# Kernel optimization log

Measured on AMD Instinct MI355X. Metric: run time of the kernel, lower is better.

Reference implementation:

```python
import jax, jax.numpy as jnp
import numpy as np

B, C, H, W = 8, 64, 32, 32
NEG = 256
TEMP = 2.0
FACTOR = 0.8
EPS = 1e-8


def setup_inputs() -> dict:
    key = jax.random.key(0)
    k1, k2, k3, k4 = jax.random.split(key, 4)
    views_1 = jax.random.normal(k1, (B, C, H, W), dtype=jnp.float32)
    views_2 = jax.random.normal(k2, (B, C, H, W), dtype=jnp.float32)
    img = jax.random.uniform(k3, (1, 3, H, W), dtype=jnp.float32)
    neg_idx = jax.random.randint(k4, (B, 2, H * W, NEG), 0, H, dtype=jnp.int32)
    return {"views_1": views_1, "views_2": views_2, "img": img, "neg_idx": neg_idx}


def _forward(views_1, views_2, img, neg_idx):
    hw = H * W
    height = jnp.arange(hw) // W
    width = jnp.arange(hw) % W
    coords = jnp.stack([height, width]).astype(jnp.float32)  # [2, hw]
    img0 = img[0]  # [3, H, W]; original uses img[0] for EVERY batch element
    euc_norm = jnp.sqrt(jnp.asarray((H - 1) ** 2 + (W - 1) ** 2, jnp.float32))
    sqrt3 = jnp.sqrt(jnp.asarray(3.0, jnp.float32))

    center = img0[:, height, width]  # [3, hw]

    def per_sample(z1, z2, nidx):
        # nidx: [2, hw, neg]
        nf = nidx.astype(jnp.float32)
        # torch.norm with no dim => scalar Frobenius norm over [2, neg] per pixel
        d = coords[:, :, None] - nf  # [2, hw, neg]
        euc = jnp.sqrt(jnp.sum(d * d, axis=(0, 2))) / euc_norm  # [hw]
        negs = img0[:, nidx[0], nidx[1]]  # [3, hw, neg]
        rd = center[:, :, None] - negs
        rgb = jnp.sqrt(jnp.sum(rd * rd, axis=(0, 2))) / sqrt3  # [hw]
        weight = euc * FACTOR + rgb * (1.0 - FACTOR)  # [hw], constant across neg

        z1v = z1.reshape(C, hw)  # [c, hw]
        pn = z2[:, nidx[0], nidx[1]]  # [c, hw, neg]
        dot = jnp.einsum('cp,cpn->pn', z1v, pn)  # [hw, neg]
        z1sq = jnp.sum(z1v * z1v, axis=0)  # [hw]
        z1n = jnp.sqrt(z1sq)
        pnn = jnp.sqrt(jnp.sum(pn * pn, axis=0))  # [hw, neg]
        cos = dot / jnp.maximum(z1n[:, None] * pnn, EPS)  # [hw, neg]
        cos0 = z1sq / jnp.maximum(z1sq, EPS)  # [hw] (self-similarity ~ 1)

        sim_neg = jnp.minimum(jnp.abs(cos * weight[:, None]), 1.0)  # [hw, neg]
        sim0 = jnp.minimum(jnp.abs(cos0), 1.0)  # [hw]
        sim = jnp.concatenate(
            [jnp.mean(sim0)[None], jnp.mean(sim_neg, axis=0) / TEMP]
        )  # [neg+1]

        # BCELoss with target = [1, 0, ..., 0]; torch clamps log terms at -100
        logp = jnp.maximum(jnp.log(sim[0]), -100.0)
        log1m = jnp.maximum(jnp.log1p(-sim[1:]), -100.0)
        bce = -(logp + jnp.sum(log1m)) / (NEG + 1)
        return bce, sim

    bce, sims = jax.vmap(per_sample)(views_1, views_2, neg_idx)
    loss = jnp.mean(bce)
    sim_all = jnp.sum(sims, axis=0)
    return (loss, sim_all[0] / B, jnp.sum(sim_all[1:]) / NEG * TEMP / B)


def reference(views_1, views_2, img, neg_idx):
    return _forward(views_1, views_2, img, neg_idx)
```

## Files before the change

### kernel.cpp

```cpp
#include <hip/hip_runtime.h>
#include <math.h>

#define BB 8
#define CC 64
#define HH 32
#define WW 32
#define HW 1024
#define NEGN 256
#define TEMP 2.0f
#define FACTOR 0.8f
#define EPSF 1e-8f

typedef short bf16x8 __attribute__((ext_vector_type(8)));
typedef float f32x4  __attribute__((ext_vector_type(4)));

__device__ inline unsigned short f2bf(float f) {
    unsigned u = __float_as_uint(f);
    u += 0x7FFFu + ((u >> 16) & 1u);
    return (unsigned short)(u >> 16);
}


__global__ __launch_bounds__(256) void prep(
    const float* __restrict__ z1,
    const float* __restrict__ z2,
    const float* __restrict__ img,
    const int*   __restrict__ nidx,
    ushort2* __restrict__ qp,
    float* __restrict__ weight_g,
    unsigned short* __restrict__ z1t,
    unsigned short* __restrict__ z2t,
    float* __restrict__ z1n_ws,
    float* __restrict__ normq_ws,
    float* __restrict__ sim0Part)
{
    __shared__ float imgs_l[3 * HW];
    __shared__ float ctile[64 * 16];
    __shared__ float csq[16];

    const int t   = threadIdx.x;
    const int blk = blockIdx.x;

    const int b_w  = blk >> 7;
    const int p0_8 = (blk & 127) * 8;
    const int lane32 = t & 31;
    const int pp_w   = t >> 5;
    const int p_w    = p0_8 + pp_w;

    const bool isZ1 = (blk < 512);
    const int cvt   = isZ1 ? blk : blk - 512;
    const int b_c   = cvt >> 6;
    const int p0c   = (cvt & 63) * 16;
    const float* __restrict__ src = isZ1 ? z1 : z2;

    const size_t nbase = ((size_t)(b_w * 2) * HW + p_w) * NEGN;
    const int2* __restrict__ nr = reinterpret_cast<const int2*>(nidx + nbase);
    const int2* __restrict__ nc =
        reinterpret_cast<const int2*>(nidx + nbase + (size_t)HW * NEGN);
    int2 rrv[4], ccv[4];
    #pragma unroll
    for (int j = 0; j < 4; ++j) {
        rrv[j] = nr[lane32 + 32 * j];
        ccv[j] = nc[lane32 + 32 * j];
    }

    {
        const float4* __restrict__ imgf4 = reinterpret_cast<const float4*>(img);
        float4* imgs4 = reinterpret_cast<float4*>(imgs_l);
        #pragma unroll
        for (int j = 0; j < 3; ++j) imgs4[t + 256 * j] = imgf4[t + 256 * j];
    }
    {
        #pragma unroll
        for (int i = 0; i < 4; ++i) {
            const int idx = t + 256 * i;
            const int c = idx >> 4, row = idx & 15;
            ctile[idx] = src[((size_t)(b_c * CC + c)) * HW + p0c + row];
        }
    }
    __syncthreads();

    {
        const float cen0 = imgs_l[p_w], cen1 = imgs_l[HW + p_w], cen2 = imgs_l[2 * HW + p_w];
        const float hp = (float)(p_w >> 5), wp = (float)(p_w & 31);

        int q[8];
        #pragma unroll
        for (int j = 0; j < 4; ++j) {
            q[2 * j]     = rrv[j].x * WW + ccv[j].x;
            q[2 * j + 1] = rrv[j].y * WW + ccv[j].y;
        }
        float g0[8], g1[8], g2[8];
        #pragma unroll
        for (int e = 0; e < 8; ++e) {
            g0[e] = imgs_l[q[e]];
            g1[e] = imgs_l[HW + q[e]];
            g2[e] = imgs_l[2 * HW + q[e]];
        }
        float se = 0.f, sr = 0.f;
        #pragma unroll
        for (int j = 0; j < 4; ++j) {
            {
                const float dh = hp - (float)rrv[j].x, dw = wp - (float)ccv[j].x;
                se += dh * dh + dw * dw;
                const float d0 = cen0 - g0[2 * j];
                const float d1 = cen1 - g1[2 * j];
                const float d2 = cen2 - g2[2 * j];
                sr += d0 * d0 + d1 * d1 + d2 * d2;
            }
            {
                const float dh = hp - (float)rrv[j].y, dw = wp - (float)ccv[j].y;
                se += dh * dh + dw * dw;
                const float d0 = cen0 - g0[2 * j + 1];
                const float d1 = cen1 - g1[2 * j + 1];
                const float d2 = cen2 - g2[2 * j + 1];
                sr += d0 * d0 + d1 * d1 + d2 * d2;
            }
        }
        #pragma unroll
        for (int off = 16; off; off >>= 1) {
            se += __shfl_xor(se, off);
            sr += __shfl_xor(sr, off);
        }
        const float euc_norm = sqrtf((float)((HH - 1) * (HH - 1) + (WW - 1) * (WW - 1)));
        const float weight = sqrtf(se) / euc_norm * FACTOR +
                             sqrtf(sr) / sqrtf(3.0f) * (1.0f - FACTOR);

        ushort2* qrow = qp + (size_t)(b_w * 1024 + p0_8) * 128;
        #pragma unroll
        for (int j = 0; j < 4; ++j)
            qrow[pp_w * 128 + lane32 + 32 * j] =
                make_ushort2((unsigned short)q[2 * j], (unsigned short)q[2 * j + 1]);
        if (lane32 == 0) weight_g[b_w * 1024 + p_w] = weight;
    }

    if (t < 16) {
        float s = 0.f;
        #pragma unroll
        for (int c = 0; c < CC; ++c) { const float v = ctile[c * 16 + t]; s += v * v; }
        if (isZ1) {
            z1n_ws[b_c * 1024 + p0c + t] = sqrtf(s);
            csq[t] = fminf(fabsf(s / fmaxf(s, EPSF)), 1.0f);
        } else {
            normq_ws[b_c * 1024 + p0c + t] = sqrtf(s);
        }
    }
    __syncthreads();
    if (isZ1 && t == 0) {
        float s0 = 0.f;
        #pragma unroll
        for (int i = 0; i < 16; ++i) s0 += csq[i];
        sim0Part[cvt] = s0;
    }

    {
        unsigned short* dst =
            (isZ1 ? z1t : z2t) + ((size_t)(b_c * 1024) + p0c) * 64;
        ushort4 pk;
        const int o = 4 * t;
        pk.x = f2bf(ctile[((o + 0) & 63) * 16 + ((o + 0) >> 6)]);
        pk.y = f2bf(ctile[((o + 1) & 63) * 16 + ((o + 1) >> 6)]);
        pk.z = f2bf(ctile[((o + 2) & 63) * 16 + ((o + 2) >> 6)]);
        pk.w = f2bf(ctile[((o + 3) & 63) * 16 + ((o + 3) >> 6)]);
        *reinterpret_cast<ushort4*>(dst + o) = pk;
    }
}

__global__ __launch_bounds__(256, 2) void gemm_mfma(
    const unsigned short* __restrict__ z1t,
    const unsigned short* __restrict__ z2t,
    const float* __restrict__ z1n_ws,
    const float* __restrict__ normq_ws,
    const ushort2* __restrict__ qp,
    const float* __restrict__ weight_g,
    float* __restrict__ simPart)
{
    __shared__ float Dt_s[16 * HW];
    __shared__ float nq_s[HW];
    __shared__ float z1n_s[16];

    const int t    = threadIdx.x;
    const int blk  = blockIdx.x;
    const int b    = blk >> 6;
    const int p0   = (blk & 63) * 16;
    const int wave = t >> 6;
    const int lane = t & 63;
    const int ln15 = lane & 15;
    const int lg   = lane >> 4;

    reinterpret_cast<float4*>(nq_s)[t] =
        reinterpret_cast<const float4*>(normq_ws + b * 1024)[t];
    if (t < 16) z1n_s[t] = z1n_ws[b * 1024 + p0 + t];

    const unsigned short* arow =
        z1t + ((size_t)(b * 1024) + p0 + ln15) * 64 + lg * 8;
    const bf16x8 a0 = *reinterpret_cast<const bf16x8*>(arow);
    const bf16x8 a1 = *reinterpret_cast<const bf16x8*>(arow + 32);

    __syncthreads();

    const int qw = wave * 256;
    #pragma unroll 4
    for (int tile = 0; tile < 16; ++tile) {
        const int q0 = qw + tile * 16;
        const unsigned short* brow =
            z2t + ((size_t)(b * 1024) + q0 + ln15) * 64 + lg * 8;
        const bf16x8 b0 = *reinterpret_cast<const bf16x8*>(brow);
        const bf16x8 b1 = *reinterpret_cast<const bf16x8*>(brow + 32);
        f32x4 acc = {0.f, 0.f, 0.f, 0.f};
        acc = __builtin_amdgcn_mfma_f32_16x16x32_bf16(a0, b0, acc, 0, 0, 0);
        acc = __builtin_amdgcn_mfma_f32_16x16x32_bf16(a1, b1, acc, 0, 0, 0);

        const float pn = nq_s[q0 + ln15];
        #pragma unroll
        for (int i = 0; i < 4; ++i) {
            const int row = lg * 4 + i;
            Dt_s[row * HW + q0 + ln15] = acc[i] / fmaxf(z1n_s[row] * pn, EPSF);
        }
    }

    const int p_b = t >> 4;
    const int tn  = t & 15;
    const ushort2* qrow = qp + (size_t)(b * 1024 + p0 + p_b) * 128;
    ushort2 qv[8];
    #pragma unroll
    for (int j = 0; j < 8; ++j) qv[j] = qrow[tn + 16 * j];
    const float weight = weight_g[b * 1024 + p0 + p_b];
    __syncthreads();

    float2 sv[8];
    #pragma unroll
    for (int j = 0; j < 8; ++j) {
        const float c0 = Dt_s[p_b * HW + qv[j].x];
        const float c1 = Dt_s[p_b * HW + qv[j].y];
        sv[j].x = fminf(fabsf(c0 * weight), 1.0f);
        sv[j].y = fminf(fabsf(c1 * weight), 1.0f);
    }
    __syncthreads();

    float2* simpart2 = reinterpret_cast<float2*>(Dt_s);
    #pragma unroll
    for (int j = 0; j < 8; ++j)
        simpart2[p_b * (NEGN / 2) + tn + 16 * j] = sv[j];
    __syncthreads();

    float s = 0.f;
    #pragma unroll
    for (int pp = 0; pp < 16; ++pp) s += Dt_s[pp * NEGN + t];
    simPart[(size_t)blk * NEGN + t] = s;
}

__global__ __launch_bounds__(256) void reduce_out(
    const float* __restrict__ simPart,
    const float* __restrict__ sim0Part,
    float* __restrict__ out)
{
    const int b = blockIdx.x;
    const int t = threadIdx.x;

    float a = 0.f;
    #pragma unroll 8
    for (int pblk = 0; pblk < 64; ++pblk)
        a += simPart[((size_t)(b * 64 + pblk)) * NEGN + t];

    const float s = a * (1.0f / HW) * (1.0f / TEMP);
    float ssum = s;
    float lsum = fmaxf(log1pf(-s), -100.0f);

    __shared__ float rs[4], rl[4];
    __shared__ float s0sh;
    #pragma unroll
    for (int off = 32; off; off >>= 1) {
        ssum += __shfl_down(ssum, off);
        lsum += __shfl_down(lsum, off);
    }
    if ((t & 63) == 0) { rs[t >> 6] = ssum; rl[t >> 6] = lsum; }

    if (t < 64) {
        float v = sim0Part[b * 64 + t];
        #pragma unroll
        for (int off = 32; off; off >>= 1) v += __shfl_xor(v, off);
        if (t == 0) s0sh = v * (1.0f / HW);
    }
    __syncthreads();

    if (t == 0) {
        const float S = rs[0] + rs[1] + rs[2] + rs[3];
        const float L = rl[0] + rl[1] + rl[2] + rl[3];
        const float s0 = s0sh;
        const float logp = fmaxf(logf(s0), -100.0f);
        atomicAdd(out + 0, -(logp + L) / ((float)(NEGN + 1) * (float)BB));
        atomicAdd(out + 1, s0 / (float)BB);
        atomicAdd(out + 2, S / (float)NEGN * TEMP / (float)BB);
    }
}

extern "C" void kernel_launch(void* const* d_in, const int* in_sizes, int n_in,
                              void* d_out, int out_size, void* d_ws, size_t ws_size,
                              hipStream_t stream) {
    const float* v1   = (const float*)d_in[0];
    const float* v2   = (const float*)d_in[1];
    const float* img  = (const float*)d_in[2];
    const int*   nidx = (const int*)  d_in[3];

    float*   simPart  = (float*)d_ws;
    float*   sim0Part = simPart + 512 * NEGN;
    float*   weight_g = sim0Part + 512;
    float*   z1n_ws   = weight_g + 8192;
    float*   normq_ws = z1n_ws + 8192;
    ushort2* qp       = (ushort2*)(normq_ws + 8192);
    unsigned short* z1t = (unsigned short*)(qp + 1048576);
    unsigned short* z2t = z1t + 8 * 1024 * 64;

    prep<<<1024, 256, 0, stream>>>(v1, v2, img, nidx, qp, weight_g,
                                   z1t, z2t, z1n_ws, normq_ws, sim0Part);
    gemm_mfma<<<512, 256, 0, stream>>>(z1t, z2t, z1n_ws, normq_ws,
                                       qp, weight_g, simPart);
    reduce_out<<<BB, 256, 0, stream>>>(simPart, sim0Part, (float*)d_out);
}
```

Baseline: 91.35 us.

## Fuse z1 prep, weight computation and final reduction into GEMM kernel

The prep kernel now only converts z2 to bf16 and computes its norms. The z1 conversion, the per-pixel distance and color weight computation from the neighbor indices, and the final loss reduction all move into the GEMM kernel. The reduction uses a last-block-done atomic counter per batch, which removes one launch and the qp/weight/z1t workspace round-trips. In exchange the GEMM kernel does more work per block and needs more registers (16 index loads held across the MFMA loop), which may reduce occupancy.

```diff
diff --git a/kernel.cpp b/kernel.cpp
--- a/kernel.cpp
+++ b/kernel.cpp
@@ -21,163 +21,63 @@
 }
 
 
-__global__ __launch_bounds__(256) void prep(
+__global__ __launch_bounds__(256) void prep_z2(
+    const float* __restrict__ z2,
+    unsigned short* __restrict__ z2t,
+    float* __restrict__ normq_ws,
+    unsigned* __restrict__ cnt)
+{
+    __shared__ float ctile[64 * 16];
+
+    const int t   = threadIdx.x;
+    const int blk = blockIdx.x;
+    const int b   = blk >> 6;
+    const int q0  = (blk & 63) * 16;
+
+    if (blk == 0 && t < 8) cnt[t] = 0;
+
+    #pragma unroll
+    for (int i = 0; i < 4; ++i) {
+        const int idx = t + 256 * i;
+        const int c = idx >> 4, row = idx & 15;
+        ctile[idx] = z2[((size_t)(b * CC + c)) * HW + q0 + row];
+    }
+    __syncthreads();
+
+    if (t < 16) {
+        float s = 0.f;
+        #pragma unroll
+        for (int c = 0; c < CC; ++c) { const float v = ctile[c * 16 + t]; s += v * v; }
+        normq_ws[b * 1024 + q0 + t] = sqrtf(s);
+    }
+
+    unsigned short* dst = z2t + ((size_t)(b * 1024) + q0) * 64;
+    ushort4 pk;
+    const int o = 4 * t;
+    pk.x = f2bf(ctile[((o + 0) & 63) * 16 + ((o + 0) >> 6)]);
+    pk.y = f2bf(ctile[((o + 1) & 63) * 16 + ((o + 1) >> 6)]);
+    pk.z = f2bf(ctile[((o + 2) & 63) * 16 + ((o + 2) >> 6)]);
+    pk.w = f2bf(ctile[((o + 3) & 63) * 16 + ((o + 3) >> 6)]);
+    *reinterpret_cast<ushort4*>(dst + o) = pk;
+}
+
+__global__ __launch_bounds__(256, 2) void gemm_fused(
     const float* __restrict__ z1,
-    const float* __restrict__ z2,
     const float* __restrict__ img,
     const int*   __restrict__ nidx,
-    ushort2* __restrict__ qp,
-    float* __restrict__ weight_g,
-    unsigned short* __restrict__ z1t,
-    unsigned short* __restrict__ z2t,
-    float* __restrict__ z1n_ws,
-    float* __restrict__ normq_ws,
-    float* __restrict__ sim0Part)
-{
-    __shared__ float imgs_l[3 * HW];
-    __shared__ float ctile[64 * 16];
-    __shared__ float csq[16];
-
-    const int t   = threadIdx.x;
-    const int blk = blockIdx.x;
-
-    const int b_w  = blk >> 7;
-    const int p0_8 = (blk & 127) * 8;
-    const int lane32 = t & 31;
-    const int pp_w   = t >> 5;
-    const int p_w    = p0_8 + pp_w;
-
-    const bool isZ1 = (blk < 512);
-    const int cvt   = isZ1 ? blk : blk - 512;
-    const int b_c   = cvt >> 6;
-    const int p0c   = (cvt & 63) * 16;
-    const float* __restrict__ src = isZ1 ? z1 : z2;
-
-    const size_t nbase = ((size_t)(b_w * 2) * HW + p_w) * NEGN;
-    const int2* __restrict__ nr = reinterpret_cast<const int2*>(nidx + nbase);
-    const int2* __restrict__ nc =
-        reinterpret_cast<const int2*>(nidx + nbase + (size_t)HW * NEGN);
-    int2 rrv[4], ccv[4];
-    #pragma unroll
-    for (int j = 0; j < 4; ++j) {
-        rrv[j] = nr[lane32 + 32 * j];
-        ccv[j] = nc[lane32 + 32 * j];
-    }
-
-    {
-        const float4* __restrict__ imgf4 = reinterpret_cast<const float4*>(img);
-        float4* imgs4 = reinterpret_cast<float4*>(imgs_l);
-        #pragma unroll
-        for (int j = 0; j < 3; ++j) imgs4[t + 256 * j] = imgf4[t + 256 * j];
-    }
-    {
-        #pragma unroll
-        for (int i = 0; i < 4; ++i) {
-            const int idx = t + 256 * i;
-            const int c = idx >> 4, row = idx & 15;
-            ctile[idx] = src[((size_t)(b_c * CC + c)) * HW + p0c + row];
-        }
-    }
-    __syncthreads();
-
-    {
-        const float cen0 = imgs_l[p_w], cen1 = imgs_l[HW + p_w], cen2 = imgs_l[2 * HW + p_w];
-        const float hp = (float)(p_w >> 5), wp = (float)(p_w & 31);
-
-        int q[8];
-        #pragma unroll
-        for (int j = 0; j < 4; ++j) {
-            q[2 * j]     = rrv[j].x * WW + ccv[j].x;
-            q[2 * j + 1] = rrv[j].y * WW + ccv[j].y;
-        }
-        float g0[8], g1[8], g2[8];
-        #pragma unroll
-        for (int e = 0; e < 8; ++e) {
-            g0[e] = imgs_l[q[e]];
-            g1[e] = imgs_l[HW + q[e]];
-            g2[e] = imgs_l[2 * HW + q[e]];
-        }
-        float se = 0.f, sr = 0.f;
-        #pragma unroll
-        for (int j = 0; j < 4; ++j) {
-            {
-                const float dh = hp - (float)rrv[j].x, dw = wp - (float)ccv[j].x;
-                se += dh * dh + dw * dw;
-                const float d0 = cen0 - g0[2 * j];
-                const float d1 = cen1 - g1[2 * j];
-                const float d2 = cen2 - g2[2 * j];
-                sr += d0 * d0 + d1 * d1 + d2 * d2;
-            }
-            {
-                const float dh = hp - (float)rrv[j].y, dw = wp - (float)ccv[j].y;
-                se += dh * dh + dw * dw;
-                const float d0 = cen0 - g0[2 * j + 1];
-                const float d1 = cen1 - g1[2 * j + 1];
-                const float d2 = cen2 - g2[2 * j + 1];
-                sr += d0 * d0 + d1 * d1 + d2 * d2;
-            }
-        }
-        #pragma unroll
-        for (int off = 16; off; off >>= 1) {
-            se += __shfl_xor(se, off);
-            sr += __shfl_xor(sr, off);
-        }
-        const float euc_norm = sqrtf((float)((HH - 1) * (HH - 1) + (WW - 1) * (WW - 1)));
-        const float weight = sqrtf(se) / euc_norm * FACTOR +
-                             sqrtf(sr) / sqrtf(3.0f) * (1.0f - FACTOR);
-
-        ushort2* qrow = qp + (size_t)(b_w * 1024 + p0_8) * 128;
-        #pragma unroll
-        for (int j = 0; j < 4; ++j)
-            qrow[pp_w * 128 + lane32 + 32 * j] =
-                make_ushort2((unsigned short)q[2 * j], (unsigned short)q[2 * j + 1]);
-        if (lane32 == 0) weight_g[b_w * 1024 + p_w] = weight;
-    }
-
-    if (t < 16) {
-        float s = 0.f;
-        #pragma unroll
-        for (int c = 0; c < CC; ++c) { const float v = ctile[c * 16 + t]; s += v * v; }
-        if (isZ1) {
-            z1n_ws[b_c * 1024 + p0c + t] = sqrtf(s);
-            csq[t] = fminf(fabsf(s / fmaxf(s, EPSF)), 1.0f);
-        } else {
-            normq_ws[b_c * 1024 + p0c + t] = sqrtf(s);
-        }
-    }
-    __syncthreads();
-    if (isZ1 && t == 0) {
-        float s0 = 0.f;
-        #pragma unroll
-        for (int i = 0; i < 16; ++i) s0 += csq[i];
-        sim0Part[cvt] = s0;
-    }
-
-    {
-        unsigned short* dst =
-            (isZ1 ? z1t : z2t) + ((size_t)(b_c * 1024) + p0c) * 64;
-        ushort4 pk;
-        const int o = 4 * t;
-        pk.x = f2bf(ctile[((o + 0) & 63) * 16 + ((o + 0) >> 6)]);
-        pk.y = f2bf(ctile[((o + 1) & 63) * 16 + ((o + 1) >> 6)]);
-        pk.z = f2bf(ctile[((o + 2) & 63) * 16 + ((o + 2) >> 6)]);
-        pk.w = f2bf(ctile[((o + 3) & 63) * 16 + ((o + 3) >> 6)]);
-        *reinterpret_cast<ushort4*>(dst + o) = pk;
-    }
-}
-
-__global__ __launch_bounds__(256, 2) void gemm_mfma(
-    const unsigned short* __restrict__ z1t,
     const unsigned short* __restrict__ z2t,
-    const float* __restrict__ z1n_ws,
     const float* __restrict__ normq_ws,
-    const ushort2* __restrict__ qp,
-    const float* __restrict__ weight_g,
-    float* __restrict__ simPart)
+    float* __restrict__ simPart,
+    float* __restrict__ sim0Part,
+    unsigned* __restrict__ cnt,
+    float* __restrict__ out)
 {
     __shared__ float Dt_s[16 * HW];
-    __shared__ float nq_s[HW];
+    __shared__ float aux[3 * HW];
     __shared__ float z1n_s[16];
+    __shared__ float z1sq_s[16];
+    __shared__ float rs[4], rl[4];
+    __shared__ int   isLast;
 
     const int t    = threadIdx.x;
     const int blk  = blockIdx.x;
@@ -188,51 +88,116 @@
     const int ln15 = lane & 15;
     const int lg   = lane >> 4;
 
+    const int p_b = t >> 4;
+    const int tn  = t & 15;
+    const size_t nbase = ((size_t)(b * 2) * HW + p0 + p_b) * NEGN;
+    const int2* __restrict__ nr = reinterpret_cast<const int2*>(nidx + nbase);
+    const int2* __restrict__ nc =
+        reinterpret_cast<const int2*>(nidx + nbase + (size_t)HW * NEGN);
+    int2 rrv[8], ccv[8];
+    #pragma unroll
+    for (int j = 0; j < 8; ++j) {
+        rrv[j] = nr[tn + 16 * j];
+        ccv[j] = nc[tn + 16 * j];
+    }
+
+    float* nq_s  = aux;
+    float* ctile = aux + HW;
     reinterpret_cast<float4*>(nq_s)[t] =
         reinterpret_cast<const float4*>(normq_ws + b * 1024)[t];
-    if (t < 16) z1n_s[t] = z1n_ws[b * 1024 + p0 + t];
-
-    const unsigned short* arow =
-        z1t + ((size_t)(b * 1024) + p0 + ln15) * 64 + lg * 8;
-    const bf16x8 a0 = *reinterpret_cast<const bf16x8*>(arow);
-    const bf16x8 a1 = *reinterpret_cast<const bf16x8*>(arow + 32);
-
+    #pragma unroll
+    for (int i = 0; i < 4; ++i) {
+        const int idx = t + 256 * i;
+        const int c = idx >> 4, row = idx & 15;
+        ctile[idx] = z1[((size_t)(b * CC + c)) * HW + p0 + row];
+    }
+    __syncthreads();
+
+    if (t < 16) {
+        float s = 0.f;
+        #pragma unroll
+        for (int c = 0; c < CC; ++c) { const float v = ctile[c * 16 + t]; s += v * v; }
+        z1sq_s[t] = s; z1n_s[t] = sqrtf(s);
+    }
+    bf16x8 a0, a1;
+    #pragma unroll
+    for (int j = 0; j < 8; ++j) {
+        a0[j] = (short)f2bf(ctile[(lg * 8 + j) * 16 + ln15]);
+        a1[j] = (short)f2bf(ctile[(32 + lg * 8 + j) * 16 + ln15]);
+    }
     __syncthreads();
 
     const int qw = wave * 256;
     #pragma unroll 4
     for (int tile = 0; tile < 16; ++tile) {
-        const int q0 = qw + tile * 16;
+        const int q0t = qw + tile * 16;
         const unsigned short* brow =
-            z2t + ((size_t)(b * 1024) + q0 + ln15) * 64 + lg * 8;
+            z2t + ((size_t)(b * 1024) + q0t + ln15) * 64 + lg * 8;
         const bf16x8 b0 = *reinterpret_cast<const bf16x8*>(brow);
         const bf16x8 b1 = *reinterpret_cast<const bf16x8*>(brow + 32);
         f32x4 acc = {0.f, 0.f, 0.f, 0.f};
         acc = __builtin_amdgcn_mfma_f32_16x16x32_bf16(a0, b0, acc, 0, 0, 0);
         acc = __builtin_amdgcn_mfma_f32_16x16x32_bf16(a1, b1, acc, 0, 0, 0);
 
-        const float pn = nq_s[q0 + ln15];
+        const float pn = nq_s[q0t + ln15];
         #pragma unroll
         for (int i = 0; i < 4; ++i) {
             const int row = lg * 4 + i;
-            Dt_s[row * HW + q0 + ln15] = acc[i] / fmaxf(z1n_s[row] * pn, EPSF);
+            Dt_s[row * HW + q0t + ln15] = acc[i] / fmaxf(z1n_s[row] * pn, EPSF);
         }
     }
-
-    const int p_b = t >> 4;
-    const int tn  = t & 15;
-    const ushort2* qrow = qp + (size_t)(b * 1024 + p0 + p_b) * 128;
-    ushort2 qv[8];
-    #pragma unroll
-    for (int j = 0; j < 8; ++j) qv[j] = qrow[tn + 16 * j];
-    const float weight = weight_g[b * 1024 + p0 + p_b];
-    __syncthreads();
+    __syncthreads();
+
+    {
+        const float4* __restrict__ imgf4 = reinterpret_cast<const float4*>(img);
+        float4* imgs4 = reinterpret_cast<float4*>(aux);
+        #pragma unroll
+        for (int j = 0; j < 3; ++j) imgs4[t + 256 * j] = imgf4[t + 256 * j];
+    }
+    __syncthreads();
+    float* imgs_l = aux;
+
+    const int pg = p0 + p_b;
+    const float cen0 = imgs_l[pg], cen1 = imgs_l[HW + pg], cen2 = imgs_l[2 * HW + pg];
+    const float hp = (float)(pg >> 5), wp = (float)(pg & 31);
+
+    int qv[16];
+    float se = 0.f, sr = 0.f;
+    #pragma unroll
+    for (int j = 0; j < 8; ++j) {
+        {
+            const int q = rrv[j].x * WW + ccv[j].x; qv[2 * j] = q;
+            const float dh = hp - (float)rrv[j].x, dw = wp - (float)ccv[j].x;
+            se += dh * dh + dw * dw;
+            const float d0 = cen0 - imgs_l[q];
+            const float d1 = cen1 - imgs_l[HW + q];
+            const float d2 = cen2 - imgs_l[2 * HW + q];
+            sr += d0 * d0 + d1 * d1 + d2 * d2;
+        }
+        {
+            const int q = rrv[j].y * WW + ccv[j].y; qv[2 * j + 1] = q;
+            const float dh = hp - (float)rrv[j].y, dw = wp - (float)ccv[j].y;
+            se += dh * dh + dw * dw;
+            const float d0 = cen0 - imgs_l[q];
+            const float d1 = cen1 - imgs_l[HW + q];
+            const float d2 = cen2 - imgs_l[2 * HW + q];
+            sr += d0 * d0 + d1 * d1 + d2 * d2;
+        }
+    }
+    #pragma unroll
+    for (int off = 8; off; off >>= 1) {
+        se += __shfl_xor(se, off);
+        sr += __shfl_xor(sr, off);
+    }
+    const float euc_norm = sqrtf((float)((HH - 1) * (HH - 1) + (WW - 1) * (WW - 1)));
+    const float weight = sqrtf(se) / euc_norm * FACTOR +
+                         sqrtf(sr) / sqrtf(3.0f) * (1.0f - FACTOR);
 
     float2 sv[8];
     #pragma unroll
     for (int j = 0; j < 8; ++j) {
-        const float c0 = Dt_s[p_b * HW + qv[j].x];
-        const float c1 = Dt_s[p_b * HW + qv[j].y];
+        const float c0 = Dt_s[p_b * HW + qv[2 * j]];
+        const float c1 = Dt_s[p_b * HW + qv[2 * j + 1]];
         sv[j].x = fminf(fabsf(c0 * weight), 1.0f);
         sv[j].y = fminf(fabsf(c1 * weight), 1.0f);
     }
@@ -248,27 +213,29 @@
     #pragma unroll
     for (int pp = 0; pp < 16; ++pp) s += Dt_s[pp * NEGN + t];
     simPart[(size_t)blk * NEGN + t] = s;
-}
-
-__global__ __launch_bounds__(256) void reduce_out(
-    const float* __restrict__ simPart,
-    const float* __restrict__ sim0Part,
-    float* __restrict__ out)
-{
-    const int b = blockIdx.x;
-    const int t = threadIdx.x;
+
+    if (t == 0) {
+        float s0 = 0.f;
+        #pragma unroll
+        for (int pp = 0; pp < 16; ++pp)
+            s0 += fminf(fabsf(z1sq_s[pp] / fmaxf(z1sq_s[pp], EPSF)), 1.0f);
+        sim0Part[blk] = s0;
+    }
+
+    __threadfence();
+    if (t == 0) isLast = (atomicAdd(&cnt[b], 1u) == 63u);
+    __syncthreads();
+    if (!isLast) return;
+    __threadfence();
 
     float a = 0.f;
     #pragma unroll 8
     for (int pblk = 0; pblk < 64; ++pblk)
         a += simPart[((size_t)(b * 64 + pblk)) * NEGN + t];
 
-    const float s = a * (1.0f / HW) * (1.0f / TEMP);
-    float ssum = s;
-    float lsum = fmaxf(log1pf(-s), -100.0f);
-
-    __shared__ float rs[4], rl[4];
-    __shared__ float s0sh;
+    const float sN = a * (1.0f / HW) * (1.0f / TEMP);
+    float ssum = sN;
+    float lsum = fmaxf(log1pf(-sN), -100.0f);
     #pragma unroll
     for (int off = 32; off; off >>= 1) {
         ssum += __shfl_down(ssum, off);
@@ -276,6 +243,7 @@
     }
     if ((t & 63) == 0) { rs[t >> 6] = ssum; rl[t >> 6] = lsum; }
 
+    __shared__ float s0sh;
     if (t < 64) {
         float v = sim0Part[b * 64 + t];
         #pragma unroll
@@ -303,18 +271,13 @@
     const float* img  = (const float*)d_in[2];
     const int*   nidx = (const int*)  d_in[3];
 
-    float*   simPart  = (float*)d_ws;
-    float*   sim0Part = simPart + 512 * NEGN;
-    float*   weight_g = sim0Part + 512;
-    float*   z1n_ws   = weight_g + 8192;
-    float*   normq_ws = z1n_ws + 8192;
-    ushort2* qp       = (ushort2*)(normq_ws + 8192);
-    unsigned short* z1t = (unsigned short*)(qp + 1048576);
-    unsigned short* z2t = z1t + 8 * 1024 * 64;
-
-    prep<<<1024, 256, 0, stream>>>(v1, v2, img, nidx, qp, weight_g,
-                                   z1t, z2t, z1n_ws, normq_ws, sim0Part);
-    gemm_mfma<<<512, 256, 0, stream>>>(z1t, z2t, z1n_ws, normq_ws,
-                                       qp, weight_g, simPart);
-    reduce_out<<<BB, 256, 0, stream>>>(simPart, sim0Part, (float*)d_out);
-}
+    float*    simPart  = (float*)d_ws;
+    float*    sim0Part = simPart + 512 * NEGN;
+    float*    normq_ws = sim0Part + 512;
+    unsigned* cnt      = (unsigned*)(normq_ws + 8192);
+    unsigned short* z2t = (unsigned short*)(cnt + 8);
+
+    prep_z2<<<512, 256, 0, stream>>>(v2, z2t, normq_ws, cnt);
+    gemm_fused<<<512, 256, 0, stream>>>(v1, img, nidx, z2t, normq_ws,
+                                        simPart, sim0Part, cnt, (float*)d_out);
+}
```

Measured after the change: 130.8 us. 43.2% more time.
